# Kernel optimization log

Hardware: AMD Instinct MI355X
Metric: run time of the kernel (lower is better)

## Reference

```python
import jax, jax.numpy as jnp
import numpy as np

HIDDEN_DIM = 2048
NUM_HEADS = 16
HEAD_DIM = HIDDEN_DIM // NUM_HEADS
BATCH = 2
SEQ = 2048


def setup_inputs() -> dict:
    key = jax.random.key(0)
    ks = jax.random.split(key, 5)
    scale = 1.0 / np.sqrt(HIDDEN_DIM)
    x = jax.random.normal(ks[0], (BATCH, SEQ, HIDDEN_DIM), dtype=jnp.float32)
    w_q = jax.random.normal(ks[1], (HIDDEN_DIM, HIDDEN_DIM), dtype=jnp.float32) * scale
    w_k = jax.random.normal(ks[2], (HIDDEN_DIM, HIDDEN_DIM), dtype=jnp.float32) * scale
    w_v = jax.random.normal(ks[3], (HIDDEN_DIM, HIDDEN_DIM), dtype=jnp.float32) * scale
    w_o = jax.random.normal(ks[4], (HIDDEN_DIM, HIDDEN_DIM), dtype=jnp.float32) * scale
    return {"x": x, "w_q": w_q, "w_k": w_k, "w_v": w_v, "w_o": w_o}


def reference(x, w_q, w_k, w_v, w_o):
    # Projections: x @ W.T  (weights stored as (out, in) like torch)
    q = jnp.einsum('bsd,ed->bse', x, w_q)
    k = jnp.einsum('bsd,ed->bse', x, w_k)
    v = jnp.einsum('bsd,ed->bse', x, w_v)
    b, s, _ = q.shape
    # split heads: (b, h, s, hd)
    q = q.reshape(b, s, NUM_HEADS, HEAD_DIM).transpose(0, 2, 1, 3)
    k = k.reshape(b, s, NUM_HEADS, HEAD_DIM).transpose(0, 2, 1, 3)
    v = v.reshape(b, s, NUM_HEADS, HEAD_DIM).transpose(0, 2, 1, 3)
    scale = 1.0 / np.sqrt(HEAD_DIM)
    # Online-softmax tiling in the source (causal=False default) is
    # mathematically identical to standard softmax attention.
    scores = jnp.einsum('bhqd,bhkd->bhqk', q, k) * scale
    p = jax.nn.softmax(scores, axis=-1)
    o = jnp.einsum('bhqk,bhkd->bhqd', p, v)
    o = o.transpose(0, 2, 1, 3).reshape(b, s, HIDDEN_DIM)
    return jnp.einsum('bsd,ed->bse', o, w_o)
```

## Files before the change

### kernel.cpp

```cpp
#include <hip/hip_runtime.h>


typedef _Float16 half8 __attribute__((ext_vector_type(8)));
typedef float floatx4 __attribute__((ext_vector_type(4)));

__device__ __forceinline__ void async16(const void* g, void* l) {
  __builtin_amdgcn_global_load_lds((__attribute__((address_space(1))) void*)(g),
                                   (__attribute__((address_space(3))) void*)(l),
                                   16, 0, 0);
}

__global__ void cvt_all(const float* __restrict__ x, const float* __restrict__ w0,
                        const float* __restrict__ w1, const float* __restrict__ w2,
                        const float* __restrict__ w3, _Float16* __restrict__ xh,
                        _Float16* __restrict__ wh, float scale0) {
  int i = blockIdx.x * blockDim.x + threadIdx.x;
  const int XQ = 1 << 21;
  float sc = 1.0f;
  const float* src;
  _Float16* dst;
  int j;
  if (i < XQ) { src = x; dst = xh; j = i; }
  else {
    int t = i - XQ;
    int m = t >> 20;
    src = (m == 0) ? w0 : (m == 1) ? w1 : (m == 2) ? w2 : w3;
    if (m == 0) sc = scale0;
    dst = wh; j = t;
  }
  int js = (i < XQ) ? j : (j & ((1 << 20) - 1));
  float4 v = reinterpret_cast<const float4*>(src)[js];
  union { _Float16 h[4]; short4 s; } u;
  u.h[0] = (_Float16)(v.x * sc); u.h[1] = (_Float16)(v.y * sc);
  u.h[2] = (_Float16)(v.z * sc); u.h[3] = (_Float16)(v.w * sc);
  reinterpret_cast<short4*>(dst)[j] = u.s;
}

template <int OUT_MODE>
__global__ __launch_bounds__(256)
void gemm_nt(const _Float16* __restrict__ A, const _Float16* __restrict__ Bw,
             void* __restrict__ Cv, void* __restrict__ Cv2, int kLen) {
  __shared__ _Float16 As[128 * 64];
  __shared__ _Float16 Bs[128 * 64];
  const int tid = threadIdx.x;
  const int wave = tid >> 6, lane = tid & 63;
  const int wm = wave >> 1, wn = wave & 1;
  const int l15 = lane & 15, l4 = lane >> 4;
  const int bm = blockIdx.y, bn = blockIdx.x;
  const int kStart = (OUT_MODE == 2) ? blockIdx.z * kLen : 0;

  floatx4 acc[4][4] = {};

  for (int k0 = kStart; k0 < kStart + kLen; k0 += 64) {
    __syncthreads();
#pragma unroll
    for (int i = 0; i < 4; ++i) {
      int c = i * 256 + tid;
      int row = c >> 3, cc = c & 7;
      int g = cc ^ (row & 7);
      async16(A + (size_t)(bm * 128 + row) * 2048 + k0 + g * 8, &As[c * 8]);
      async16(Bw + (size_t)(bn * 128 + row) * 2048 + k0 + g * 8, &Bs[c * 8]);
    }
    __syncthreads();
#pragma unroll
    for (int ks = 0; ks < 2; ++ks) {
      half8 af[4], bf[4];
      int ch = (ks * 4 + l4) ^ (l15 & 7);
#pragma unroll
      for (int t = 0; t < 4; ++t) {
        af[t] = *reinterpret_cast<const half8*>(&As[(wm * 64 + t * 16 + l15) * 64 + ch * 8]);
        bf[t] = *reinterpret_cast<const half8*>(&Bs[(wn * 64 + t * 16 + l15) * 64 + ch * 8]);
      }
#pragma unroll
      for (int mt = 0; mt < 4; ++mt)
#pragma unroll
        for (int nt = 0; nt < 4; ++nt)
          acc[mt][nt] = __builtin_amdgcn_mfma_f32_16x16x32_f16(af[mt], bf[nt], acc[mt][nt], 0, 0, 0);
    }
  }

  const int rbase = bm * 128 + wm * 64;
  const int cbase = bn * 128 + wn * 64;
  if constexpr (OUT_MODE == 0) {
    if (cbase < 4096) {
      _Float16* C = (_Float16*)Cv + (size_t)(cbase >> 11) * (4096ull * 2048);
#pragma unroll
      for (int mt = 0; mt < 4; ++mt)
#pragma unroll
        for (int nt = 0; nt < 4; ++nt) {
          int r0 = rbase + mt * 16 + l4 * 4;
          int cg = (cbase + nt * 16 + l15) & 2047;
#pragma unroll
          for (int r = 0; r < 4; ++r)
            C[(size_t)(r0 + r) * 2048 + cg] = (_Float16)acc[mt][nt][r];
        }
    } else {
      _Float16* C = (_Float16*)Cv2;
#pragma unroll
      for (int mt = 0; mt < 4; ++mt)
#pragma unroll
        for (int nt = 0; nt < 4; ++nt) {
          int m0 = rbase + mt * 16 + l4 * 4;
          int d = cbase + nt * 16 + l15 - 4096;
          size_t base = (size_t)(m0 >> 11) * (2048ull * 2048) + (size_t)d * 2048 + (m0 & 2047);
          union { _Float16 h[4]; short4 s; } u;
#pragma unroll
          for (int r = 0; r < 4; ++r) u.h[r] = (_Float16)acc[mt][nt][r];
          *reinterpret_cast<short4*>(C + base) = u.s;
        }
    }
  } else {
    float* C = (float*)Cv + (size_t)blockIdx.z * 8388608ull;
#pragma unroll
    for (int mt = 0; mt < 4; ++mt)
#pragma unroll
      for (int nt = 0; nt < 4; ++nt) {
        int r0 = rbase + mt * 16 + l4 * 4;
        int cg = cbase + nt * 16 + l15;
#pragma unroll
        for (int r = 0; r < 4; ++r)
          C[(size_t)(r0 + r) * 2048 + cg] = acc[mt][nt][r];
      }
  }
}

__global__ void reduce_add(const float* __restrict__ p, float* __restrict__ out) {
  int i = blockIdx.x * blockDim.x + threadIdx.x;
  float4 a = reinterpret_cast<const float4*>(p)[i];
  float4 b = reinterpret_cast<const float4*>(p + 8388608)[i];
  float4 o; o.x = a.x + b.x; o.y = a.y + b.y; o.z = a.z + b.z; o.w = a.w + b.w;
  reinterpret_cast<float4*>(out)[i] = o;
}

__global__ __launch_bounds__(256, 2)
void flash_attn(const _Float16* __restrict__ Q, const _Float16* __restrict__ Kg,
                const _Float16* __restrict__ Vt, _Float16* __restrict__ O) {
  __shared__ _Float16 Ks[64 * 128];
  __shared__ _Float16 Vs[128 * 64];
  __shared__ _Float16 Ps[128 * 64];
  const int tid = threadIdx.x, wave = tid >> 6, lane = tid & 63;
  const int l15 = lane & 15, l4 = lane >> 4;
  const int bh = blockIdx.y, b = bh >> 4, h = bh & 15;
  const int q0 = blockIdx.x * 128;

  const _Float16* Qp = Q + ((size_t)(b * 2048 + q0 + wave * 32)) * 2048 + h * 128;
  const _Float16* Kp = Kg + (size_t)b * 2048 * 2048 + h * 128;
  const _Float16* Vp = Vt + (size_t)b * 2048 * 2048 + (size_t)(h * 128) * 2048;

  half8 qf[2][4];
#pragma unroll
  for (int mt = 0; mt < 2; ++mt)
#pragma unroll
    for (int ks = 0; ks < 4; ++ks)
      qf[mt][ks] = *reinterpret_cast<const half8*>(
          Qp + (size_t)(mt * 16 + l15) * 2048 + ks * 32 + l4 * 8);

  floatx4 oacc[2][8] = {};
  float lsum[2][4] = {};

  for (int k0 = 0; k0 < 2048; k0 += 64) {
    __syncthreads();
#pragma unroll
    for (int i = 0; i < 4; ++i) {
      int c = i * 256 + tid;
      int row = c >> 4, cc = c & 15;
      int g = cc ^ (row & 15);
      async16(Kp + (size_t)(k0 + row) * 2048 + g * 8, &Ks[c * 8]);
    }
#pragma unroll
    for (int i = 0; i < 4; ++i) {
      int c = i * 256 + tid;
      int row = c >> 3, cc = c & 7;
      int g = cc ^ (row & 7);
      async16(Vp + (size_t)row * 2048 + k0 + g * 8, &Vs[c * 8]);
    }
    __syncthreads();

    floatx4 sacc[2][4] = {};
#pragma unroll
    for (int ks = 0; ks < 4; ++ks) {
      half8 bf[4];
#pragma unroll
      for (int nt = 0; nt < 4; ++nt) {
        int row = nt * 16 + l15;
        int ch = (ks * 4 + l4) ^ l15;
        bf[nt] = *reinterpret_cast<const half8*>(&Ks[row * 128 + ch * 8]);
      }
#pragma unroll
      for (int mt = 0; mt < 2; ++mt)
#pragma unroll
        for (int nt = 0; nt < 4; ++nt)
          sacc[mt][nt] = __builtin_amdgcn_mfma_f32_16x16x32_f16(qf[mt][ks], bf[nt], sacc[mt][nt], 0, 0, 0);
    }

#pragma unroll
    for (int mt = 0; mt < 2; ++mt)
#pragma unroll
      for (int nt = 0; nt < 4; ++nt)
#pragma unroll
        for (int r = 0; r < 4; ++r) {
          float p = exp2f(sacc[mt][nt][r]);
          lsum[mt][r] += p;
          int rl = l4 * 4 + r;
          int ch = (nt * 2 + (l15 >> 3)) ^ (rl & 7);
          Ps[(wave * 32 + mt * 16 + rl) * 64 + ch * 8 + (l15 & 7)] = (_Float16)p;
        }

    __builtin_amdgcn_s_waitcnt(0xC07F);

#pragma unroll
    for (int ks2 = 0; ks2 < 2; ++ks2) {
      half8 pf[2];
#pragma unroll
      for (int mt = 0; mt < 2; ++mt)
        pf[mt] = *reinterpret_cast<const half8*>(
            &Ps[(wave * 32 + mt * 16 + l15) * 64 + (((ks2 * 4 + l4) ^ (l15 & 7)) * 8)]);
#pragma unroll
      for (int nt2 = 0; nt2 < 8; ++nt2) {
        int row = nt2 * 16 + l15;
        int ch = (ks2 * 4 + l4) ^ (row & 7);
        half8 vf = *reinterpret_cast<const half8*>(&Vs[row * 64 + ch * 8]);
#pragma unroll
        for (int mt = 0; mt < 2; ++mt)
          oacc[mt][nt2] = __builtin_amdgcn_mfma_f32_16x16x32_f16(pf[mt], vf, oacc[mt][nt2], 0, 0, 0);
      }
    }
  }

#pragma unroll
  for (int mt = 0; mt < 2; ++mt)
#pragma unroll
    for (int r = 0; r < 4; ++r) {
#pragma unroll
      for (int off = 1; off < 16; off <<= 1) lsum[mt][r] += __shfl_xor(lsum[mt][r], off);
    }

  _Float16* Op = O + ((size_t)(b * 2048 + q0 + wave * 32)) * 2048 + h * 128;
#pragma unroll
  for (int mt = 0; mt < 2; ++mt)
#pragma unroll
    for (int r = 0; r < 4; ++r) {
      float inv = 1.0f / lsum[mt][r];
#pragma unroll
      for (int nt2 = 0; nt2 < 8; ++nt2) {
        int row = mt * 16 + l4 * 4 + r;
        int col = nt2 * 16 + l15;
        Op[(size_t)row * 2048 + col] = (_Float16)(oacc[mt][nt2][r] * inv);
      }
    }
}

extern "C" void kernel_launch(void* const* d_in, const int* in_sizes, int n_in,
                              void* d_out, int out_size, void* d_ws, size_t ws_size,
                              hipStream_t stream) {
  const float* x = (const float*)d_in[0];
  const float* wq = (const float*)d_in[1];
  const float* wk = (const float*)d_in[2];
  const float* wv = (const float*)d_in[3];
  const float* wo = (const float*)d_in[4];
  float* out = (float*)d_out;

  const size_t XN = (size_t)4096 * 2048;
  const size_t WN = (size_t)2048 * 2048;
  _Float16* xh = (_Float16*)d_ws;
  _Float16* qh = xh + XN;
  _Float16* vth = xh + 3 * XN;
  _Float16* oh = xh + 4 * XN;
  _Float16* wqh = xh + 5 * XN;
  float* pparts = (float*)d_ws;

  const float SM_SCALE = 0.08838834764831845f * 1.4426950408889634f;

  cvt_all<<<dim3(24576), 256, 0, stream>>>(x, wq, wk, wv, wo, xh, wqh, SM_SCALE);
  gemm_nt<0><<<dim3(48, 32), 256, 0, stream>>>(xh, wqh, qh, vth, 2048);
  flash_attn<<<dim3(16, 32), 256, 0, stream>>>(qh, qh + XN, vth, oh);
  gemm_nt<2><<<dim3(16, 32, 2), 256, 0, stream>>>(oh, wqh + 3 * WN, pparts, nullptr, 1024);
  reduce_add<<<dim3(8192), 256, 0, stream>>>(pparts, out);
}
```

Before: 424.2 us.

## Drop split-K output GEMM and transpose score MFMA for vectorized P stores

```diff
diff --git a/kernel.cpp b/kernel.cpp
--- a/kernel.cpp
+++ b/kernel.cpp
@@ -2,6 +2,7 @@
 
 
 typedef _Float16 half8 __attribute__((ext_vector_type(8)));
+typedef _Float16 half4 __attribute__((ext_vector_type(4)));
 typedef float floatx4 __attribute__((ext_vector_type(4)));
 
 __device__ __forceinline__ void async16(const void* g, void* l) {
@@ -39,7 +40,7 @@
 template <int OUT_MODE>
 __global__ __launch_bounds__(256)
 void gemm_nt(const _Float16* __restrict__ A, const _Float16* __restrict__ Bw,
-             void* __restrict__ Cv, void* __restrict__ Cv2, int kLen) {
+             void* __restrict__ Cv, void* __restrict__ Cv2) {
   __shared__ _Float16 As[128 * 64];
   __shared__ _Float16 Bs[128 * 64];
   const int tid = threadIdx.x;
@@ -47,11 +48,10 @@
   const int wm = wave >> 1, wn = wave & 1;
   const int l15 = lane & 15, l4 = lane >> 4;
   const int bm = blockIdx.y, bn = blockIdx.x;
-  const int kStart = (OUT_MODE == 2) ? blockIdx.z * kLen : 0;
 
   floatx4 acc[4][4] = {};
 
-  for (int k0 = kStart; k0 < kStart + kLen; k0 += 64) {
+  for (int k0 = 0; k0 < 2048; k0 += 64) {
     __syncthreads();
 #pragma unroll
     for (int i = 0; i < 4; ++i) {
@@ -110,7 +110,7 @@
         }
     }
   } else {
-    float* C = (float*)Cv + (size_t)blockIdx.z * 8388608ull;
+    float* C = (float*)Cv;
 #pragma unroll
     for (int mt = 0; mt < 4; ++mt)
 #pragma unroll
@@ -122,14 +122,6 @@
           C[(size_t)(r0 + r) * 2048 + cg] = acc[mt][nt][r];
       }
   }
-}
-
-__global__ void reduce_add(const float* __restrict__ p, float* __restrict__ out) {
-  int i = blockIdx.x * blockDim.x + threadIdx.x;
-  float4 a = reinterpret_cast<const float4*>(p)[i];
-  float4 b = reinterpret_cast<const float4*>(p + 8388608)[i];
-  float4 o; o.x = a.x + b.x; o.y = a.y + b.y; o.z = a.z + b.z; o.w = a.w + b.w;
-  reinterpret_cast<float4*>(out)[i] = o;
 }
 
 __global__ __launch_bounds__(256, 2)
@@ -149,14 +141,14 @@
 
   half8 qf[2][4];
 #pragma unroll
-  for (int mt = 0; mt < 2; ++mt)
+  for (int qt = 0; qt < 2; ++qt)
 #pragma unroll
     for (int ks = 0; ks < 4; ++ks)
-      qf[mt][ks] = *reinterpret_cast<const half8*>(
-          Qp + (size_t)(mt * 16 + l15) * 2048 + ks * 32 + l4 * 8);
+      qf[qt][ks] = *reinterpret_cast<const half8*>(
+          Qp + (size_t)(qt * 16 + l15) * 2048 + ks * 32 + l4 * 8);
 
   floatx4 oacc[2][8] = {};
-  float lsum[2][4] = {};
+  float lsumq[2] = {0.f, 0.f};
 
   for (int k0 = 0; k0 < 2048; k0 += 64) {
     __syncthreads();
@@ -176,35 +168,39 @@
     }
     __syncthreads();
 
-    floatx4 sacc[2][4] = {};
+    floatx4 sacc[4][2] = {};
 #pragma unroll
     for (int ks = 0; ks < 4; ++ks) {
-      half8 bf[4];
-#pragma unroll
-      for (int nt = 0; nt < 4; ++nt) {
-        int row = nt * 16 + l15;
+      half8 kf[4];
+#pragma unroll
+      for (int st = 0; st < 4; ++st) {
+        int row = st * 16 + l15;
         int ch = (ks * 4 + l4) ^ l15;
-        bf[nt] = *reinterpret_cast<const half8*>(&Ks[row * 128 + ch * 8]);
-      }
-#pragma unroll
-      for (int mt = 0; mt < 2; ++mt)
-#pragma unroll
-        for (int nt = 0; nt < 4; ++nt)
-          sacc[mt][nt] = __builtin_amdgcn_mfma_f32_16x16x32_f16(qf[mt][ks], bf[nt], sacc[mt][nt], 0, 0, 0);
-    }
-
-#pragma unroll
-    for (int mt = 0; mt < 2; ++mt)
-#pragma unroll
-      for (int nt = 0; nt < 4; ++nt)
-#pragma unroll
-        for (int r = 0; r < 4; ++r) {
-          float p = exp2f(sacc[mt][nt][r]);
-          lsum[mt][r] += p;
-          int rl = l4 * 4 + r;
-          int ch = (nt * 2 + (l15 >> 3)) ^ (rl & 7);
-          Ps[(wave * 32 + mt * 16 + rl) * 64 + ch * 8 + (l15 & 7)] = (_Float16)p;
-        }
+        kf[st] = *reinterpret_cast<const half8*>(&Ks[row * 128 + ch * 8]);
+      }
+#pragma unroll
+      for (int st = 0; st < 4; ++st)
+#pragma unroll
+        for (int qt = 0; qt < 2; ++qt)
+          sacc[st][qt] = __builtin_amdgcn_mfma_f32_16x16x32_f16(kf[st], qf[qt][ks], sacc[st][qt], 0, 0, 0);
+    }
+
+#pragma unroll
+    for (int qt = 0; qt < 2; ++qt)
+#pragma unroll
+      for (int st = 0; st < 4; ++st) {
+        float p0 = exp2f(sacc[st][qt][0]);
+        float p1 = exp2f(sacc[st][qt][1]);
+        float p2 = exp2f(sacc[st][qt][2]);
+        float p3 = exp2f(sacc[st][qt][3]);
+        lsumq[qt] += (p0 + p1) + (p2 + p3);
+        half4 pv;
+        pv[0] = (_Float16)p0; pv[1] = (_Float16)p1;
+        pv[2] = (_Float16)p2; pv[3] = (_Float16)p3;
+        int ch = (st * 2 + (l4 >> 1)) ^ (l15 & 7);
+        *reinterpret_cast<half4*>(
+            &Ps[(wave * 32 + qt * 16 + l15) * 64 + ch * 8 + (l4 & 1) * 4]) = pv;
+      }
 
     __builtin_amdgcn_s_waitcnt(0xC07F);
 
@@ -228,19 +224,17 @@
   }
 
 #pragma unroll
+  for (int qt = 0; qt < 2; ++qt) {
+    lsumq[qt] += __shfl_xor(lsumq[qt], 16);
+    lsumq[qt] += __shfl_xor(lsumq[qt], 32);
+  }
+
+  _Float16* Op = O + ((size_t)(b * 2048 + q0 + wave * 32)) * 2048 + h * 128;
+#pragma unroll
   for (int mt = 0; mt < 2; ++mt)
 #pragma unroll
     for (int r = 0; r < 4; ++r) {
-#pragma unroll
-      for (int off = 1; off < 16; off <<= 1) lsum[mt][r] += __shfl_xor(lsum[mt][r], off);
-    }
-
-  _Float16* Op = O + ((size_t)(b * 2048 + q0 + wave * 32)) * 2048 + h * 128;
-#pragma unroll
-  for (int mt = 0; mt < 2; ++mt)
-#pragma unroll
-    for (int r = 0; r < 4; ++r) {
-      float inv = 1.0f / lsum[mt][r];
+      float inv = 1.0f / __shfl(lsumq[mt], l4 * 4 + r);
 #pragma unroll
       for (int nt2 = 0; nt2 < 8; ++nt2) {
         int row = mt * 16 + l4 * 4 + r;
@@ -267,13 +261,11 @@
   _Float16* vth = xh + 3 * XN;
   _Float16* oh = xh + 4 * XN;
   _Float16* wqh = xh + 5 * XN;
-  float* pparts = (float*)d_ws;
 
   const float SM_SCALE = 0.08838834764831845f * 1.4426950408889634f;
 
   cvt_all<<<dim3(24576), 256, 0, stream>>>(x, wq, wk, wv, wo, xh, wqh, SM_SCALE);
-  gemm_nt<0><<<dim3(48, 32), 256, 0, stream>>>(xh, wqh, qh, vth, 2048);
+  gemm_nt<0><<<dim3(48, 32), 256, 0, stream>>>(xh, wqh, qh, vth);
   flash_attn<<<dim3(16, 32), 256, 0, stream>>>(qh, qh + XN, vth, oh);
-  gemm_nt<2><<<dim3(16, 32, 2), 256, 0, stream>>>(oh, wqh + 3 * WN, pparts, nullptr, 1024);
-  reduce_add<<<dim3(8192), 256, 0, stream>>>(pparts, out);
-}
+  gemm_nt<2><<<dim3(16, 32), 256, 0, stream>>>(oh, wqh + 3 * WN, out, nullptr);
+}
```

New measurement: 396.8 us. 6.5% less time.
